# Kernel optimization log

Hardware: AMD Instinct MI355X
Metric: run time of the kernel (lower is better)

## Reference

```python
import jax, jax.numpy as jnp
import numpy as np

IOU_TR = 0.3
SCORE_TR = 0.1
EPS = 1e-9
N_DET = 4096
N_CLASSES = 20


def setup_inputs() -> dict:
    key = jax.random.key(0)
    k1, k2, k3, k4 = jax.random.split(key, 4)
    scores = jax.random.uniform(k1, (N_DET,), dtype=jnp.float32)
    classes = jax.random.randint(k2, (N_DET,), 0, N_CLASSES).astype(jnp.float32)
    centers = jax.random.uniform(k3, (N_DET, 3), dtype=jnp.float32) * 64.0
    dims = jax.random.uniform(k4, (N_DET, 3), dtype=jnp.float32) * 8.0 + 1.0
    results = jnp.concatenate([scores[:, None], classes[:, None], centers, dims], axis=1)
    return {"results": results}


def _pairwise_iou3d(boxes):
    # boxes: [N, 6] = (cx, cy, cz, w, h, d) center format
    c = boxes[:, :3]
    d = boxes[:, 3:]
    lo = c - d * 0.5  # [N,3]
    hi = c + d * 0.5
    inter_lo = jnp.maximum(lo[:, None, :], lo[None, :, :])  # [N,N,3]
    inter_hi = jnp.minimum(hi[:, None, :], hi[None, :, :])
    inter = jnp.prod(jnp.clip(inter_hi - inter_lo, 0.0, None), axis=-1)  # [N,N]
    vol = jnp.prod(d, axis=-1)  # [N]
    union = vol[:, None] + vol[None, :] - inter
    return inter / (union + EPS)


def reference(results):
    # results: [N, 8] = (score, class, cx, cy, cz, w, h, d)
    N = results.shape[0]
    order = jnp.argsort(-results[:, 0])  # sort by score descending
    r = results[order]
    valid = r[:, 0] >= SCORE_TR  # score threshold filter
    iou = _pairwise_iou3d(r[:, 2:])  # [N,N]
    idx = jnp.arange(N)

    def body(i, state):
        keep, active = state
        cur = active[i]
        keep = keep.at[i].set(cur)
        # suppress later boxes whose IoU with box i exceeds threshold
        sup = cur & (iou[i] > IOU_TR) & (idx > i)
        active = active & (~sup)
        return keep, active

    keep, _ = jax.lax.fori_loop(0, N, body, (jnp.zeros(N, dtype=bool), valid))
    # static-shape output: suppressed / filtered rows zeroed instead of compacted
    return jnp.where(keep[:, None], r, jnp.zeros_like(r))
```

## Files before the change

kernel.cpp:

```cpp
#include <hip/hip_runtime.h>

typedef unsigned long long u64;
typedef unsigned int u32;
typedef unsigned short u16;

#define N_DET 4096
#define NW 64
#define IOU_TR 0.3f
#define SCORE_TR 0.1f
#define EPS 1e-9f


__device__ __forceinline__ u64 rl64(u64 v, int l) {
    unsigned lo = __builtin_amdgcn_readlane((unsigned)v, l);
    unsigned hi = __builtin_amdgcn_readlane((unsigned)(v >> 32), l);
    return ((u64)hi << 32) | lo;
}

__global__ void __launch_bounds__(256) k_sort(const float* __restrict__ res,
                                              float* __restrict__ rows,
                                              float* __restrict__ ssc,
                                              float4* __restrict__ soaLO,
                                              float4* __restrict__ soaHI,
                                              u64* __restrict__ A,
                                              u64* __restrict__ Trm) {
    __shared__ float s[N_DET];
    int tid = threadIdx.x;
    if (blockIdx.x == 0) {
        if (tid < 64) A[tid] = 0ull;
        if (tid >= 64 && tid < 128)
            Trm[(size_t)4095 * NW + (tid - 64)] = 0ull;
    }
    for (int j = tid; j < N_DET; j += 256) s[j] = res[j * 8];
    __syncthreads();
    int r = tid >> 4, c = tid & 15;
    int gi = blockIdx.x * 16 + r;
    float sc = s[gi];
    int part = 0;
    int j0 = c * 256;
    for (int j = j0; j < j0 + 256; ++j) {
        float sj = s[j];
        part += (sj > sc) || (sj == sc && j < gi);
    }
    part += __shfl_xor(part, 1, 64);
    part += __shfl_xor(part, 2, 64);
    part += __shfl_xor(part, 4, 64);
    part += __shfl_xor(part, 8, 64);
    if (c == 0) {
        int rank = part;
        float4 a = *(const float4*)(res + gi * 8);
        float4 b = *(const float4*)(res + gi * 8 + 4);
        *(float4*)(rows + rank * 8)     = a;
        *(float4*)(rows + rank * 8 + 4) = b;
        ssc[rank] = a.x;
        float cx = a.z, cy = a.w, cz = b.x, dx = b.y, dy = b.z, dz = b.w;
        soaLO[rank] = make_float4(cx - dx * 0.5f, cy - dy * 0.5f,
                                  cz - dz * 0.5f, (dx * dy) * dz);
        soaHI[rank] = make_float4(cx + dx * 0.5f, cy + dy * 0.5f,
                                  cz + dz * 0.5f, 0.0f);
    }
}

__global__ void k_sup(const float4* __restrict__ soaLO,
                      const float4* __restrict__ soaHI,
                      const float* __restrict__ ssc,
                      u64* __restrict__ Trm, u64* __restrict__ A) {
    int lane = threadIdx.x & 63;
    int wave = threadIdx.x >> 6;
    int i = blockIdx.x * 4 + wave;
    if (ssc[i] < SCORE_TR) return;
    float4 iLO = soaLO[i];
    float4 iHI = soaHI[i];
    u64 rowword = 0, rowOr = 0;
    for (int w = (i >> 6); w < NW; ++w) {
        int j = w * 64 + lane;
        float4 jLO = soaLO[j];
        float4 jHI = soaHI[j];
        float ix = fminf(iHI.x, jHI.x) - fmaxf(iLO.x, jLO.x); ix = fmaxf(ix, 0.f);
        float iy = fminf(iHI.y, jHI.y) - fmaxf(iLO.y, jLO.y); iy = fmaxf(iy, 0.f);
        float iz = fminf(iHI.z, jHI.z) - fmaxf(iLO.z, jLO.z); iz = fmaxf(iz, 0.f);
        float inter = (ix * iy) * iz;
        float uni = iLO.w + jLO.w - inter;
        float iou = inter / (uni + EPS);
        bool sb = (iou > IOU_TR) && (j > i);
        u64 m = __ballot(sb);
        rowOr |= m;
        rowword = (lane == w) ? m : rowword;
    }
    if (rowOr) {
        Trm[(size_t)i * NW + lane] = rowword;
        if (lane == 0) atomicOr(&A[i >> 6], 1ull << (i & 63));
    }
}

#define FIDX(V, GB) { V = (u32)s_nlist[(GB) + (lane & 15)]; }

#define IS1(V, P, S) { u32 si_ = (u32)__builtin_amdgcn_readlane((V), (S)); \
    P##S = Trm[(size_t)si_ * NW + lane]; }

#define IS16(V, P) IS1(V,P,0) IS1(V,P,1) IS1(V,P,2) IS1(V,P,3)   \
    IS1(V,P,4) IS1(V,P,5) IS1(V,P,6) IS1(V,P,7)                  \
    IS1(V,P,8) IS1(V,P,9) IS1(V,P,10) IS1(V,P,11)                \
    IS1(V,P,12) IS1(V,P,13) IS1(V,P,14) IS1(V,P,15)

#define PR1(V, P, S) { u32 si_ = (u32)__builtin_amdgcn_readlane((V), (S)); \
    u64 awd_ = rl64(act, (int)(si_ >> 6));                                 \
    u64 m_ = 0ull - ((awd_ >> (si_ & 63u)) & 1ull);                        \
    act &= ~(P##S & m_); }

#define PR16(V, P) PR1(V,P,0) PR1(V,P,1) PR1(V,P,2) PR1(V,P,3)   \
    PR1(V,P,4) PR1(V,P,5) PR1(V,P,6) PR1(V,P,7)                  \
    PR1(V,P,8) PR1(V,P,9) PR1(V,P,10) PR1(V,P,11)                \
    PR1(V,P,12) PR1(V,P,13) PR1(V,P,14) PR1(V,P,15)

__global__ void __launch_bounds__(256, 1)
k_scan(const u64* __restrict__ Trm, const u64* __restrict__ A,
       const float* __restrict__ ssc, u64* __restrict__ keep) {
    __shared__ u64 s_valid[NW];
    __shared__ u16 s_nlist[4352];
    const int tid = threadIdx.x;
    const int wv = tid >> 6;
    const int lane = tid & 63;

    for (int w = wv * 16; w < wv * 16 + 16; ++w) {
        float scw = ssc[w * 64 + lane];
        u64 m = __ballot(scw >= SCORE_TR);
        if (lane == 0) s_valid[w] = m;
    }
    __syncthreads();
    if (wv != 0) return;

    u64 act = s_valid[lane];
    u64 avA = A[lane] & act;
    int pc = __popcll(avA);
    int inc = pc;
#pragma unroll
    for (int d = 1; d < 64; d <<= 1) {
        int t = __shfl_up(inc, d, 64);
        if (lane >= d) inc += t;
    }
    int exc = inc - pc;
    int nTotal = __shfl(inc, 63, 64);
    {
        u64 m = avA; int o = exc;
        while (m) {
            int k = __builtin_ctzll(m); m &= m - 1;
            s_nlist[o++] = (u16)(lane * 64 + k);
        }
    }
    int padded = (nTotal + 63) & ~63;
    for (int t = nTotal + lane; t < padded + 192; t += 64)
        s_nlist[t] = (u16)4095;
    __threadfence_block();

    if (padded > 0) {
        u64 pa0,pa1,pa2,pa3,pa4,pa5,pa6,pa7,
            pa8,pa9,pa10,pa11,pa12,pa13,pa14,pa15;
        u64 pb0,pb1,pb2,pb3,pb4,pb5,pb6,pb7,
            pb8,pb9,pb10,pb11,pb12,pb13,pb14,pb15;
        u64 pc0,pc1,pc2,pc3,pc4,pc5,pc6,pc7,
            pc8,pc9,pc10,pc11,pc12,pc13,pc14,pc15;
        u64 pd0,pd1,pd2,pd3,pd4,pd5,pd6,pd7,
            pd8,pd9,pd10,pd11,pd12,pd13,pd14,pd15;
        u32 iA, iB, iC, iD;
        FIDX(iA, 0)  IS16(iA, pa)
        FIDX(iB, 16) IS16(iB, pb)
        FIDX(iC, 32) IS16(iC, pc)
        int g = 0;
        while (g < padded) {
            FIDX(iD, g + 48)  PR16(iA, pa)  IS16(iD, pd)
            FIDX(iA, g + 64)  PR16(iB, pb)  IS16(iA, pa)
            FIDX(iB, g + 80)  PR16(iC, pc)  IS16(iB, pb)
            FIDX(iC, g + 96)  PR16(iD, pd)  IS16(iC, pc)
            g += 64;
        }
    }
    keep[lane] = act;
}

__global__ void k_out(const float* __restrict__ rows,
                      const u64* __restrict__ keep,
                      float* __restrict__ out) {
    int i = blockIdx.x * 256 + threadIdx.x;
    bool kp = (keep[i >> 6] >> (i & 63)) & 1ull;
    float4 a = kp ? ((const float4*)rows)[i * 2]     : make_float4(0.f, 0.f, 0.f, 0.f);
    float4 b = kp ? ((const float4*)rows)[i * 2 + 1] : make_float4(0.f, 0.f, 0.f, 0.f);
    ((float4*)out)[i * 2]     = a;
    ((float4*)out)[i * 2 + 1] = b;
}

extern "C" void kernel_launch(void* const* d_in, const int* in_sizes, int n_in,
                              void* d_out, int out_size, void* d_ws, size_t ws_size,
                              hipStream_t stream) {
    const float* res = (const float*)d_in[0];
    float* out = (float*)d_out;

    float*  rows  = (float*)d_ws;
    float*  ssc   = rows + N_DET * 8;
    float4* soaLO = (float4*)(ssc + N_DET);
    float4* soaHI = soaLO + N_DET;
    u64*    A     = (u64*)(soaHI + N_DET);
    u64*    keep  = A + NW;
    u64*    Trm   = keep + NW;

    k_sort<<<N_DET / 16, 256, 0, stream>>>(res, rows, ssc, soaLO, soaHI, A, Trm);
    k_sup <<<N_DET / 4, 256, 0, stream>>>(soaLO, soaHI, ssc, Trm, A);
    k_scan<<<1, 256, 0, stream>>>(Trm, A, ssc, keep);
    k_out <<<16, 256, 0, stream>>>(rows, keep, out);
}
```

Measured before the change: 55.31 us.

## Use producer waves to prefetch suppression rows into LDS for the serial scan

The single-wave scan that kept four register-resident batches of 16 prefetched rows is restructured. Waves 1-3 now act as producers, each loading 16 suppression-mask rows per step into a double-buffered LDS staging area (48 rows per step). Wave 0 consumes the staged rows serially to update the active mask. The aim is to hide global-load latency behind more loaders and to drop the large register footprint. In exchange, every 48-row step now pays a block-wide __syncthreads and extra LDS reads on the critical path.

```diff
diff --git a/kernel.cpp b/kernel.cpp
--- a/kernel.cpp
+++ b/kernel.cpp
@@ -93,31 +93,13 @@
     }
 }
 
-#define FIDX(V, GB) { V = (u32)s_nlist[(GB) + (lane & 15)]; }
-
-#define IS1(V, P, S) { u32 si_ = (u32)__builtin_amdgcn_readlane((V), (S)); \
-    P##S = Trm[(size_t)si_ * NW + lane]; }
-
-#define IS16(V, P) IS1(V,P,0) IS1(V,P,1) IS1(V,P,2) IS1(V,P,3)   \
-    IS1(V,P,4) IS1(V,P,5) IS1(V,P,6) IS1(V,P,7)                  \
-    IS1(V,P,8) IS1(V,P,9) IS1(V,P,10) IS1(V,P,11)                \
-    IS1(V,P,12) IS1(V,P,13) IS1(V,P,14) IS1(V,P,15)
-
-#define PR1(V, P, S) { u32 si_ = (u32)__builtin_amdgcn_readlane((V), (S)); \
-    u64 awd_ = rl64(act, (int)(si_ >> 6));                                 \
-    u64 m_ = 0ull - ((awd_ >> (si_ & 63u)) & 1ull);                        \
-    act &= ~(P##S & m_); }
-
-#define PR16(V, P) PR1(V,P,0) PR1(V,P,1) PR1(V,P,2) PR1(V,P,3)   \
-    PR1(V,P,4) PR1(V,P,5) PR1(V,P,6) PR1(V,P,7)                  \
-    PR1(V,P,8) PR1(V,P,9) PR1(V,P,10) PR1(V,P,11)                \
-    PR1(V,P,12) PR1(V,P,13) PR1(V,P,14) PR1(V,P,15)
-
 __global__ void __launch_bounds__(256, 1)
 k_scan(const u64* __restrict__ Trm, const u64* __restrict__ A,
        const float* __restrict__ ssc, u64* __restrict__ keep) {
     __shared__ u64 s_valid[NW];
-    __shared__ u16 s_nlist[4352];
+    __shared__ u16 s_nlist[4608];
+    __shared__ int s_nsb;
+    __shared__ u64 sbuf[2][48][64];
     const int tid = threadIdx.x;
     const int wv = tid >> 6;
     const int lane = tid & 63;
@@ -128,54 +110,67 @@
         if (lane == 0) s_valid[w] = m;
     }
     __syncthreads();
-    if (wv != 0) return;
-
-    u64 act = s_valid[lane];
-    u64 avA = A[lane] & act;
-    int pc = __popcll(avA);
-    int inc = pc;
-#pragma unroll
-    for (int d = 1; d < 64; d <<= 1) {
-        int t = __shfl_up(inc, d, 64);
-        if (lane >= d) inc += t;
-    }
-    int exc = inc - pc;
-    int nTotal = __shfl(inc, 63, 64);
-    {
+
+    if (wv == 0) {
+        u64 avA = A[lane] & s_valid[lane];
+        int pc = __popcll(avA);
+        int inc = pc;
+#pragma unroll
+        for (int d = 1; d < 64; d <<= 1) {
+            int t = __shfl_up(inc, d, 64);
+            if (lane >= d) inc += t;
+        }
+        int exc = inc - pc;
+        int nTotal = __shfl(inc, 63, 64);
         u64 m = avA; int o = exc;
         while (m) {
             int k = __builtin_ctzll(m); m &= m - 1;
             s_nlist[o++] = (u16)(lane * 64 + k);
         }
-    }
-    int padded = (nTotal + 63) & ~63;
-    for (int t = nTotal + lane; t < padded + 192; t += 64)
-        s_nlist[t] = (u16)4095;
-    __threadfence_block();
-
-    if (padded > 0) {
-        u64 pa0,pa1,pa2,pa3,pa4,pa5,pa6,pa7,
-            pa8,pa9,pa10,pa11,pa12,pa13,pa14,pa15;
-        u64 pb0,pb1,pb2,pb3,pb4,pb5,pb6,pb7,
-            pb8,pb9,pb10,pb11,pb12,pb13,pb14,pb15;
-        u64 pc0,pc1,pc2,pc3,pc4,pc5,pc6,pc7,
-            pc8,pc9,pc10,pc11,pc12,pc13,pc14,pc15;
-        u64 pd0,pd1,pd2,pd3,pd4,pd5,pd6,pd7,
-            pd8,pd9,pd10,pd11,pd12,pd13,pd14,pd15;
-        u32 iA, iB, iC, iD;
-        FIDX(iA, 0)  IS16(iA, pa)
-        FIDX(iB, 16) IS16(iB, pb)
-        FIDX(iC, 32) IS16(iC, pc)
-        int g = 0;
-        while (g < padded) {
-            FIDX(iD, g + 48)  PR16(iA, pa)  IS16(iD, pd)
-            FIDX(iA, g + 64)  PR16(iB, pb)  IS16(iA, pa)
-            FIDX(iB, g + 80)  PR16(iC, pc)  IS16(iB, pb)
-            FIDX(iC, g + 96)  PR16(iD, pd)  IS16(iC, pc)
-            g += 64;
-        }
-    }
-    keep[lane] = act;
+        int nSB = (nTotal + 47) / 48;
+        for (int t = nTotal + lane; t < (nSB + 1) * 48; t += 64)
+            s_nlist[t] = (u16)4095;
+        if (lane == 0) s_nsb = nSB;
+    }
+    __syncthreads();
+
+    const int nSB = s_nsb;
+    if (wv > 0 && nSB > 0) {
+        const int base = (wv - 1) * 16;
+#pragma unroll
+        for (int s = 0; s < 16; ++s) {
+            u32 si = (u32)s_nlist[base + s];
+            sbuf[0][base + s][lane] = Trm[(size_t)si * NW + lane];
+        }
+    }
+    u64 act = s_valid[lane];
+    __syncthreads();
+
+    for (int t = 0; t < nSB; ++t) {
+        const int cur = t & 1;
+        if (wv > 0) {
+            const int base = (wv - 1) * 16;
+            const int off = (t + 1) * 48 + base;
+#pragma unroll
+            for (int s = 0; s < 16; ++s) {
+                u32 si = (u32)s_nlist[off + s];
+                sbuf[cur ^ 1][base + s][lane] = Trm[(size_t)si * NW + lane];
+            }
+        } else {
+            const int off = t * 48;
+#pragma unroll
+            for (int s = 0; s < 48; ++s) {
+                u32 siv = (u32)s_nlist[off + s];
+                u32 si = (u32)__builtin_amdgcn_readfirstlane((int)siv);
+                u64 row = sbuf[cur][s][lane];
+                u64 aw = rl64(act, (int)(si >> 6));
+                u64 msk = 0ull - ((aw >> (si & 63u)) & 1ull);
+                act &= ~(row & msk);
+            }
+        }
+        __syncthreads();
+    }
+    if (wv == 0) keep[lane] = act;
 }
 
 __global__ void k_out(const float* __restrict__ rows,
```

Measured after the change: 52.50 us. -5.1%, faster.
